# Kernel tuning notes

Measured on AMD Instinct MI355X. Metric: run time of the kernel, lower is better.

## Reference

```python
import jax, jax.numpy as jnp
import numpy as np

POOLING_COUNTS = [15, 8, 8]
N = 128
D = 256
B = 16


def _build_specs():
    # Replicates the (kernel, stride, i, j) schedule of SparseConv.__init__.
    specs = []
    stride, offset = 1, 0
    for ci, c in enumerate(POOLING_COUNTS):
        for k in range(c):
            offset += stride
            i = np.arange(0, N - offset, stride)
            j = np.arange(offset, N, stride)
            kern = 3 if (ci > 0 and k == 0) else 2  # first conv of later groups downsamples
            st = 2 if (ci > 0 and k == 0) else 1
            specs.append((kern, st, i, j))
        stride *= 2
    return specs

SPECS = _build_specs()
N_K2 = sum(1 for s in SPECS if s[0] == 2)  # 29 kernel-2 stride-1 convs
N_K3 = sum(1 for s in SPECS if s[0] == 3)  # 2 kernel-3 stride-2 convs


def _conv1d(x, w, b, stride):
    # x: (B, D, L), w: (O, I, K) -> (B, O, L_out), VALID padding like nn.Conv1d
    y = jax.lax.conv_general_dilated(x, w, (stride,), 'VALID',
                                     dimension_numbers=('NCH', 'OIH', 'NCH'))
    return y + b[None, :, None]


def setup_inputs() -> dict:
    key = jax.random.key(0)
    ks = jax.random.split(key, 5)
    scale = 1.0 / np.sqrt(2.0 * D)  # ~ PyTorch Conv1d default init scale
    return {
        'x': jax.random.normal(ks[0], (B, D, N), jnp.float32),
        'w2': jax.random.normal(ks[1], (N_K2, D, D, 2), jnp.float32) * scale,
        'b2': jax.random.normal(ks[2], (N_K2, D), jnp.float32) * scale,
        'w3': jax.random.normal(ks[3], (N_K3, D, D, 3), jnp.float32) * scale,
        'b3': jax.random.normal(ks[4], (N_K3, D), jnp.float32) * scale,
    }


def reference(x, w2, b2, w3, b3):
    diag = np.arange(N)
    # map2d[:, :, i, i] = x
    map2d = jnp.zeros((B, D, N, N), x.dtype).at[:, :, diag, diag].set(x)
    c2 = c3 = 0
    for kern, st, i, j in SPECS:  # fixed-length chain of 31 structurally distinct convs
        if kern == 2:
            x = _conv1d(x, w2[c2], b2[c2], 1)
            c2 += 1
        else:
            x = _conv1d(x, w3[c3], b3[c3], 2)
            c3 += 1
        map2d = map2d.at[:, :, i, j].set(x)  # scatter stripe into sparse 2D map
    return map2d
```

## Files before the change

### kernel.cpp

```cpp
#include <hip/hip_runtime.h>

typedef __bf16 bf16x8 __attribute__((ext_vector_type(8)));
typedef float  floatx4 __attribute__((ext_vector_type(4)));
typedef float  fvec4  __attribute__((ext_vector_type(4)));
typedef unsigned short ushort4v __attribute__((ext_vector_type(4)));

__device__ __forceinline__ unsigned short f2bf(float f) {
  unsigned int u = __float_as_uint(f);
  u = u + 0x7FFFu + ((u >> 16) & 1u);
  return (unsigned short)(u >> 16);
}

__device__ __forceinline__ void gload_lds16(const unsigned short* g, unsigned short* l) {
  __builtin_amdgcn_global_load_lds(
      (const __attribute__((address_space(1))) unsigned int*)(g),
      (__attribute__((address_space(3))) unsigned int*)(l), 16, 0, 0);
}

#define WP3_OFF   3801088
#define XC0_E     8388608
#define TBL_E     47185920
#define Y_B       100663296

__global__ __launch_bounds__(256) void prep_kernel(
    const float* __restrict__ w2, const float* __restrict__ w3,
    const float* __restrict__ x, unsigned short* __restrict__ ws)
{
  int g = blockIdx.x * 256 + threadIdx.x;
  if (g < 1048576) {
    const float* src; unsigned short* dst;
    if (g < 950272) { src = w2; dst = ws; }
    else            { g -= 950272; src = w3; dst = ws + WP3_OFF; }
    fvec4 v = *reinterpret_cast<const fvec4*>(src + 4 * g);
    ushort4v o;
    o[0] = f2bf(v[0]); o[1] = f2bf(v[1]); o[2] = f2bf(v[2]); o[3] = f2bf(v[3]);
    *reinterpret_cast<ushort4v*>(dst + 4 * g) = o;
  } else {
    const int h = g - 1048576;
    const long f = (long)4 * h;
    const int bb = (int)(f >> 15);
    const int i  = (int)((f >> 7) & 255);
    const int p0 = (int)(f & 127);
    fvec4 v = *reinterpret_cast<const fvec4*>(x + f);
    unsigned short* xb = ws + XC0_E + (long)bb * 65536;
#pragma unroll
    for (int j = 0; j < 4; ++j) {
      const int p = p0 + j;
      const unsigned short bf = f2bf(v[j]);
      xb[p * 512 + ((2 * i) ^ ((p & 7) << 3))] = bf;
      if (p >= 1) xb[(p - 1) * 512 + ((2 * i + 1) ^ (((p - 1) & 7) << 3))] = bf;
    }
  }
}

__global__ __launch_bounds__(256) void tbl_kernel(unsigned short* __restrict__ tbl)
{
  const int g = blockIdx.x * 256 + threadIdx.x;
  const int h = g >> 13, rl = (g >> 7) & 63, c = g & 127;
  const int r = h * 64 + rl, d = c - r;
  unsigned short v = 0xFFFFu;
  if (d == 0) v = (unsigned short)(31 * 65 + rl);
  else if (d >= 1 && d <= 15) v = (unsigned short)((d - 1) * 65 + rl);
  else if (d >= 17 && d <= 31 && (d & 1) == 1 && (r & 1) == 0)
    v = (unsigned short)((15 + ((d - 17) >> 1)) * 65 + (rl >> 1));
  else if (d >= 35 && d <= 63 && (d & 3) == 3 && (r & 3) == 0)
    v = (unsigned short)((23 + ((d - 35) >> 2)) * 65 + (rl >> 2));
  tbl[g] = v;
}

template<int KW, int KWN>
__global__ __launch_bounds__(256) void conv_kernel(
    const unsigned short* __restrict__ Xin,
    unsigned short* __restrict__ Xout,
    const unsigned short* __restrict__ WP,
    const float* __restrict__ bias,
    float* __restrict__ Yl,
    int Lout)
{
  constexpr int WROW  = 256 * KW;
  constexpr int BSTR  = (KW == 2) ? 65536 : 49152;
  constexpr int BSTRN = (KWN == 3) ? 49152 : 65536;
  constexpr int KS    = 256 * KW;
  constexpr int NLD   = (KW == 2) ? 8 : 12;
  __shared__ unsigned short LA[32 * WROW];

  const int tid = threadIdx.x, wave = tid >> 6, lane = tid & 63;
  const int b = blockIdx.z, m0 = blockIdx.x * 32, n0 = blockIdx.y * 64;

  {
    const unsigned short* src = Xin + (long)b * BSTR + (long)m0 * WROW
                              + wave * (NLD * 512) + lane * 8;
    unsigned short* dst = &LA[wave * (NLD * 512)];
#pragma unroll
    for (int v = 0; v < NLD; ++v)
      gload_lds16(src + v * 512, dst + v * 512);
  }
  __syncthreads();

  const int l15 = lane & 15, quad = lane >> 4;
  const int nn = n0 + wave * 16 + l15;
  const float bv = bias[nn];
  const unsigned short* wrow = WP + (long)nn * KS + quad * 8;
  const int sx = (l15 & 7) << 3;

  floatx4 acc0 = {0.f, 0.f, 0.f, 0.f};
  floatx4 acc1 = {0.f, 0.f, 0.f, 0.f};
#pragma unroll
  for (int kc = 0; kc < KS / 32; ++kc) {
    bf16x8 bfrag = *reinterpret_cast<const bf16x8*>(wrow + kc * 32);
    const int ko = (quad * 8 + kc * 32) ^ sx;
    bf16x8 a0 = *reinterpret_cast<const bf16x8*>(&LA[l15 * WROW + ko]);
    bf16x8 a1 = *reinterpret_cast<const bf16x8*>(&LA[(16 + l15) * WROW + ko]);
    acc0 = __builtin_amdgcn_mfma_f32_16x16x32_bf16(a0, bfrag, acc0, 0, 0, 0);
    acc1 = __builtin_amdgcn_mfma_f32_16x16x32_bf16(a1, bfrag, acc1, 0, 0, 0);
  }

  const int row = b * 256 + nn;
  float* yo = Yl + (long)row * 128;
  unsigned short* xb = (KWN != 0) ? (Xout + (long)b * BSTRN) : (unsigned short*)0;
#pragma unroll
  for (int half = 0; half < 2; ++half) {
    const floatx4& A = half ? acc1 : acc0;
#pragma unroll
    for (int r = 0; r < 4; ++r) {
      const int m = m0 + half * 16 + quad * 4 + r;
      if (m < Lout) {
        const float v = A[r] + bv;
        yo[m] = v;
        const unsigned short bf = f2bf(v);
        if constexpr (KWN == 2) {
          xb[m * 512 + ((2 * nn) ^ ((m & 7) << 3))] = bf;
          if (m >= 1) xb[(m - 1) * 512 + ((2 * nn + 1) ^ (((m - 1) & 7) << 3))] = bf;
        } else if constexpr (KWN == 3) {
          if ((m & 1) == 0) {
            const int mh = m >> 1;
            xb[mh * 768 + ((3 * nn) ^ ((mh & 7) << 3))] = bf;
            if (m >= 2) xb[(mh - 1) * 768 + ((3 * nn + 2) ^ (((mh - 1) & 7) << 3))] = bf;
          } else {
            const int mh = m >> 1;
            xb[mh * 768 + ((3 * nn + 1) ^ ((mh & 7) << 3))] = bf;
          }
        }
      }
    }
  }
}

__global__ __launch_bounds__(256) void assemble_kernel(
    float* __restrict__ out, const float* __restrict__ x,
    const unsigned short* __restrict__ tbl, const float* __restrict__ Y)
{
  __shared__ float S[32 * 65];
  const int bh = blockIdx.x;
  const int blk = bh >> 1, h = bh & 1;
  const int tid = threadIdx.x;

  ushort4v t4s[8];
  const unsigned short* tb = tbl + h * 8192;
#pragma unroll
  for (int it = 0; it < 8; ++it)
    t4s[it] = *reinterpret_cast<const ushort4v*>(tb + 4 * (it * 256 + tid));

#pragma unroll
  for (int p = 0; p < 8; ++p) {
    const int idx = p * 256 + tid;
    const int slot = idx >> 6, m = idx & 63;
    if (slot < 15) {
      const int mm = h * 64 + m;
      if (mm < 127 - slot) S[slot * 65 + m] = Y[(long)slot * 524288 + blk * 128 + mm];
    } else if (slot < 23) {
      if (m < 32) {
        const int mm = h * 32 + m;
        const int Lout = (slot == 15) ? 56 : (71 - slot);
        if (mm < Lout) S[slot * 65 + m] = Y[(long)slot * 524288 + blk * 128 + mm];
      }
    } else if (slot < 31) {
      if (m < 16) {
        const int mm = h * 16 + m;
        const int Lout = (slot == 23) ? 24 : (47 - slot);
        if (mm < Lout) S[slot * 65 + m] = Y[(long)slot * 524288 + blk * 128 + mm];
      }
    } else {
      S[31 * 65 + m] = x[blk * 128 + h * 64 + m];
    }
  }
  __syncthreads();

  const long obase = ((long)blk << 14) + ((long)h << 13);
#pragma unroll
  for (int it = 0; it < 8; ++it) {
    const int flat = it * 256 + tid;
    const ushort4v t4 = t4s[it];
    fvec4 v;
#pragma unroll
    for (int jj = 0; jj < 4; ++jj) {
      const unsigned short t = t4[jj];
      const int idx = (t == 0xFFFFu) ? 0 : (int)t;
      const float sv = S[idx];
      v[jj] = (t == 0xFFFFu) ? 0.f : sv;
    }
    *reinterpret_cast<fvec4*>(out + obase + 4 * flat) = v;
  }
}

extern "C" void kernel_launch(void* const* d_in, const int* in_sizes, int n_in,
                              void* d_out, int out_size, void* d_ws, size_t ws_size,
                              hipStream_t stream)
{
  const float* x  = (const float*)d_in[0];
  const float* w2 = (const float*)d_in[1];
  const float* b2 = (const float*)d_in[2];
  const float* w3 = (const float*)d_in[3];
  const float* b3 = (const float*)d_in[4];
  float* out = (float*)d_out;
  unsigned short* ws = (unsigned short*)d_ws;
  unsigned short* tbl = ws + TBL_E;
  float* Y = (float*)((char*)d_ws + Y_B);

  prep_kernel<<<4608, 256, 0, stream>>>(w2, w3, x, ws);
  tbl_kernel<<<64, 256, 0, stream>>>(tbl);

  long cin = XC0_E;
  int Lin = 128;
  int c2 = 0, c3 = 0;
  for (int l = 0; l < 31; ++l) {
    const int KW = (l == 15 || l == 23) ? 3 : 2;
    const int cs = (KW == 3) ? 2 : 1;
    const int Lout = (Lin - KW) / cs + 1;
    const int KWN = (l == 30) ? 0 : ((l == 14 || l == 22) ? 3 : 2);
    const long cnext = cin + (long)16 * ((KW == 2) ? 65536 : 49152);
    const unsigned short* WPt; const float* bt;
    if (KW == 2) { WPt = ws + (long)c2 * 131072; bt = b2 + c2 * 256; ++c2; }
    else         { WPt = ws + WP3_OFF + (long)c3 * 196608; bt = b3 + c3 * 256; ++c3; }
    dim3 grid((Lout + 31) / 32, 4, 16);
    float* Yl = Y + (long)l * 524288;
    if (KW == 2 && KWN == 2)
      conv_kernel<2,2><<<grid, 256, 0, stream>>>(ws + cin, ws + cnext, WPt, bt, Yl, Lout);
    else if (KW == 2 && KWN == 3)
      conv_kernel<2,3><<<grid, 256, 0, stream>>>(ws + cin, ws + cnext, WPt, bt, Yl, Lout);
    else if (KW == 3 && KWN == 2)
      conv_kernel<3,2><<<grid, 256, 0, stream>>>(ws + cin, ws + cnext, WPt, bt, Yl, Lout);
    else
      conv_kernel<2,0><<<grid, 256, 0, stream>>>(ws + cin, (unsigned short*)0, WPt, bt, Yl, Lout);
    cin = cnext;
    Lin = Lout;
  }

  assemble_kernel<<<8192, 256, 0, stream>>>(out, x, tbl, Y);
}
```

Baseline: 523.7 us.

## Fuse the last sixteen conv layers into one persistent per-batch kernel

The 16 conv layers after the first downsampling move into one kernel with one block per batch element. Each block keeps its activations in a ping-pong LDS arena and walks through all remaining layers, reading weights straight from global memory. This removes 16 kernel launches and the global round-trips of intermediate activations. In exchange, only 16 workgroups run and the weights are re-fetched per block without LDS tiling, so the tail runs with very low parallelism.

```diff
diff --git a/kernel.cpp b/kernel.cpp
--- a/kernel.cpp
+++ b/kernel.cpp
@@ -19,6 +19,7 @@
 
 #define WP3_OFF   3801088
 #define XC0_E     8388608
+#define C15_E     24117248
 #define TBL_E     47185920
 #define Y_B       100663296
 
@@ -70,12 +71,9 @@
 
 template<int KW, int KWN>
 __global__ __launch_bounds__(256) void conv_kernel(
-    const unsigned short* __restrict__ Xin,
-    unsigned short* __restrict__ Xout,
-    const unsigned short* __restrict__ WP,
-    const float* __restrict__ bias,
-    float* __restrict__ Yl,
-    int Lout)
+    const unsigned short* __restrict__ Xin, unsigned short* __restrict__ Xout,
+    const unsigned short* __restrict__ WP, const float* __restrict__ bias,
+    float* __restrict__ Yl, int Lout)
 {
   constexpr int WROW  = 256 * KW;
   constexpr int BSTR  = (KW == 2) ? 65536 : 49152;
@@ -86,7 +84,6 @@
 
   const int tid = threadIdx.x, wave = tid >> 6, lane = tid & 63;
   const int b = blockIdx.z, m0 = blockIdx.x * 32, n0 = blockIdx.y * 64;
-
   {
     const unsigned short* src = Xin + (long)b * BSTR + (long)m0 * WROW
                               + wave * (NLD * 512) + lane * 8;
@@ -132,18 +129,123 @@
           xb[m * 512 + ((2 * nn) ^ ((m & 7) << 3))] = bf;
           if (m >= 1) xb[(m - 1) * 512 + ((2 * nn + 1) ^ (((m - 1) & 7) << 3))] = bf;
         } else if constexpr (KWN == 3) {
+          const int mh = m >> 1;
           if ((m & 1) == 0) {
-            const int mh = m >> 1;
             xb[mh * 768 + ((3 * nn) ^ ((mh & 7) << 3))] = bf;
             if (m >= 2) xb[(mh - 1) * 768 + ((3 * nn + 2) ^ (((mh - 1) & 7) << 3))] = bf;
           } else {
-            const int mh = m >> 1;
             xb[mh * 768 + ((3 * nn + 1) ^ ((mh & 7) << 3))] = bf;
           }
         }
       }
     }
   }
+}
+
+template<int KW, int KWN, int LOUT>
+__device__ __forceinline__ void tail_step(
+    unsigned short* __restrict__ arena, const int inOff, const int outOff,
+    const unsigned short* __restrict__ WP, const float* __restrict__ bias,
+    float* __restrict__ Yl, int b, int tid)
+{
+  constexpr int KS = 256 * KW, WROW = KS;
+  constexpr int MT = (LOUT + 15) / 16;
+  const int wave = tid >> 6, lane = tid & 63, l15 = lane & 15, quad = lane >> 4;
+  const int sx = (l15 & 7) << 3;
+
+#pragma unroll
+  for (int nt = 0; nt < 4; ++nt) {
+    const int nn = nt * 64 + wave * 16 + l15;
+    const unsigned short* wrow = WP + (long)nn * KS + quad * 8;
+    const float bv = bias[nn];
+    const int row = b * 256 + nn;
+    float* yo = Yl + (long)row * 128;
+#pragma unroll
+    for (int mt = 0; mt < MT; mt += 2) {
+      floatx4 acc0 = {0.f, 0.f, 0.f, 0.f};
+      floatx4 acc1 = {0.f, 0.f, 0.f, 0.f};
+#pragma unroll
+      for (int kc = 0; kc < KS / 32; ++kc) {
+        bf16x8 bfrag = *reinterpret_cast<const bf16x8*>(wrow + kc * 32);
+        const int ko = (quad * 8 + kc * 32) ^ sx;
+        bf16x8 a0 = *reinterpret_cast<const bf16x8*>(&arena[inOff + (mt * 16 + l15) * WROW + ko]);
+        bf16x8 a1 = *reinterpret_cast<const bf16x8*>(&arena[inOff + ((mt + 1) * 16 + l15) * WROW + ko]);
+        acc0 = __builtin_amdgcn_mfma_f32_16x16x32_bf16(a0, bfrag, acc0, 0, 0, 0);
+        acc1 = __builtin_amdgcn_mfma_f32_16x16x32_bf16(a1, bfrag, acc1, 0, 0, 0);
+      }
+#pragma unroll
+      for (int half = 0; half < 2; ++half) {
+        const floatx4& A = half ? acc1 : acc0;
+#pragma unroll
+        for (int r = 0; r < 4; ++r) {
+          const int m = (mt + half) * 16 + quad * 4 + r;
+          if (m < LOUT) {
+            const float v = A[r] + bv;
+            yo[m] = v;
+            const unsigned short bf = f2bf(v);
+            if constexpr (KWN == 2) {
+              arena[outOff + m * 512 + ((2 * nn) ^ ((m & 7) << 3))] = bf;
+              if (m >= 1)
+                arena[outOff + (m - 1) * 512 + ((2 * nn + 1) ^ (((m - 1) & 7) << 3))] = bf;
+            } else if constexpr (KWN == 3) {
+              const int mh = m >> 1;
+              if ((m & 1) == 0) {
+                arena[outOff + mh * 768 + ((3 * nn) ^ ((mh & 7) << 3))] = bf;
+                if (m >= 2)
+                  arena[outOff + (mh - 1) * 768 + ((3 * nn + 2) ^ (((mh - 1) & 7) << 3))] = bf;
+              } else {
+                arena[outOff + mh * 768 + ((3 * nn + 1) ^ ((mh & 7) << 3))] = bf;
+              }
+            }
+          }
+        }
+      }
+    }
+  }
+  __syncthreads();
+}
+
+#define R0 0
+#define R1 43776
+__global__ __launch_bounds__(256) void tail_kernel(
+    const unsigned short* __restrict__ ws,
+    const float* __restrict__ b2, const float* __restrict__ b3,
+    float* __restrict__ Y)
+{
+  __shared__ unsigned short arena[76800];
+  const int tid = threadIdx.x, b = blockIdx.x;
+  const int wave = tid >> 6, lane = tid & 63;
+
+  {
+    const unsigned short* src = ws + C15_E + (long)b * 49152;
+#pragma unroll
+    for (int it = 0; it < 21; ++it) {
+      const int base = it * 256 + wave * 64;
+      gload_lds16(src + (base + lane) * 8, &arena[base * 8]);
+    }
+  }
+  __syncthreads();
+
+  const unsigned short* wp2 = ws;
+  const unsigned short* wp3 = ws + WP3_OFF;
+  float* Yl = Y + (long)15 * 524288;
+
+  tail_step<3,2,56>(arena, R0, R1, wp3,               b3,             Yl, b, tid); Yl += 524288;
+  tail_step<2,2,55>(arena, R1, R0, wp2 + 15L*131072,  b2 + 15*256,    Yl, b, tid); Yl += 524288;
+  tail_step<2,2,54>(arena, R0, R1, wp2 + 16L*131072,  b2 + 16*256,    Yl, b, tid); Yl += 524288;
+  tail_step<2,2,53>(arena, R1, R0, wp2 + 17L*131072,  b2 + 17*256,    Yl, b, tid); Yl += 524288;
+  tail_step<2,2,52>(arena, R0, R1, wp2 + 18L*131072,  b2 + 18*256,    Yl, b, tid); Yl += 524288;
+  tail_step<2,2,51>(arena, R1, R0, wp2 + 19L*131072,  b2 + 19*256,    Yl, b, tid); Yl += 524288;
+  tail_step<2,2,50>(arena, R0, R1, wp2 + 20L*131072,  b2 + 20*256,    Yl, b, tid); Yl += 524288;
+  tail_step<2,3,49>(arena, R1, R0, wp2 + 21L*131072,  b2 + 21*256,    Yl, b, tid); Yl += 524288;
+  tail_step<3,2,24>(arena, R0, R1, wp3 + 196608,      b3 + 256,       Yl, b, tid); Yl += 524288;
+  tail_step<2,2,23>(arena, R1, R0, wp2 + 22L*131072,  b2 + 22*256,    Yl, b, tid); Yl += 524288;
+  tail_step<2,2,22>(arena, R0, R1, wp2 + 23L*131072,  b2 + 23*256,    Yl, b, tid); Yl += 524288;
+  tail_step<2,2,21>(arena, R1, R0, wp2 + 24L*131072,  b2 + 24*256,    Yl, b, tid); Yl += 524288;
+  tail_step<2,2,20>(arena, R0, R1, wp2 + 25L*131072,  b2 + 25*256,    Yl, b, tid); Yl += 524288;
+  tail_step<2,2,19>(arena, R1, R0, wp2 + 26L*131072,  b2 + 26*256,    Yl, b, tid); Yl += 524288;
+  tail_step<2,2,18>(arena, R0, R1, wp2 + 27L*131072,  b2 + 27*256,    Yl, b, tid); Yl += 524288;
+  tail_step<2,0,17>(arena, R1, R0, wp2 + 28L*131072,  b2 + 28*256,    Yl, b, tid);
 }
 
 __global__ __launch_bounds__(256) void assemble_kernel(
@@ -222,29 +324,22 @@
 
   long cin = XC0_E;
   int Lin = 128;
-  int c2 = 0, c3 = 0;
-  for (int l = 0; l < 31; ++l) {
-    const int KW = (l == 15 || l == 23) ? 3 : 2;
-    const int cs = (KW == 3) ? 2 : 1;
-    const int Lout = (Lin - KW) / cs + 1;
-    const int KWN = (l == 30) ? 0 : ((l == 14 || l == 22) ? 3 : 2);
-    const long cnext = cin + (long)16 * ((KW == 2) ? 65536 : 49152);
-    const unsigned short* WPt; const float* bt;
-    if (KW == 2) { WPt = ws + (long)c2 * 131072; bt = b2 + c2 * 256; ++c2; }
-    else         { WPt = ws + WP3_OFF + (long)c3 * 196608; bt = b3 + c3 * 256; ++c3; }
+  for (int l = 0; l < 15; ++l) {
+    const int Lout = Lin - 1;
+    const long cnext = cin + (long)16 * 65536;
+    const unsigned short* WPt = ws + (long)l * 131072;
+    const float* bt = b2 + l * 256;
     dim3 grid((Lout + 31) / 32, 4, 16);
     float* Yl = Y + (long)l * 524288;
-    if (KW == 2 && KWN == 2)
+    if (l == 14)
+      conv_kernel<2,3><<<grid, 256, 0, stream>>>(ws + cin, ws + cnext, WPt, bt, Yl, Lout);
+    else
       conv_kernel<2,2><<<grid, 256, 0, stream>>>(ws + cin, ws + cnext, WPt, bt, Yl, Lout);
-    else if (KW == 2 && KWN == 3)
-      conv_kernel<2,3><<<grid, 256, 0, stream>>>(ws + cin, ws + cnext, WPt, bt, Yl, Lout);
-    else if (KW == 3 && KWN == 2)
-      conv_kernel<3,2><<<grid, 256, 0, stream>>>(ws + cin, ws + cnext, WPt, bt, Yl, Lout);
-    else
-      conv_kernel<2,0><<<grid, 256, 0, stream>>>(ws + cin, (unsigned short*)0, WPt, bt, Yl, Lout);
     cin = cnext;
     Lin = Lout;
   }
 
+  tail_kernel<<<16, 256, 0, stream>>>(ws, b2, b3, Y);
+
   assemble_kernel<<<8192, 256, 0, stream>>>(out, x, tbl, Y);
 }
```

After: 799.5 us. 1.53x slower.
